# Optimization experiments

Measured on AMD Instinct MI355X. Metric: run time of the kernel, lower is better.

Reference implementation:

```python
import jax, jax.numpy as jnp
import numpy as np

HIDDEN, NH, NKV, HD = 2048, 16, 2, 128
CTX, NL, POS = 4096, 36, 3000
THETA, EPS = 1.0e6, 1e-6


def _rope_cos_sin(pos):
    inv_freq = 1.0 / (THETA ** (jnp.arange(0, HD, 2, dtype=jnp.float32) / HD))  # [HD/2]
    ang = pos * inv_freq
    ang = jnp.concatenate([ang, ang])  # [HD]
    return jnp.cos(ang), jnp.sin(ang)


def _rotate_half(x):
    x1, x2 = x[..., : HD // 2], x[..., HD // 2 :]
    return jnp.concatenate([-x2, x1], axis=-1)


def setup_inputs() -> dict:
    key = jax.random.key(0)
    ks = jax.random.split(key, 12)
    w = lambda k, shape, s=0.02: (jax.random.normal(k, shape, dtype=jnp.float32) * s)
    mask = jnp.where(jnp.arange(CTX) <= POS, 0.0, -1e9).astype(jnp.float32).reshape(1, 1, 1, CTX)
    return {
        "hidden_states": jax.random.normal(ks[0], (1, 1, HIDDEN), dtype=jnp.float32),
        "position_ids": jnp.array([POS], dtype=jnp.int64 if jax.config.jax_enable_x64 else jnp.int32),
        "causal_mask": mask,
        "current_pos": POS,
        "ln_w": jnp.ones((HIDDEN,), jnp.float32) + w(ks[1], (HIDDEN,)),
        "wq": w(ks[2], (NH * HD, HIDDEN)),
        "bq": w(ks[3], (NH * HD,)),
        "wk": w(ks[4], (NKV * HD, HIDDEN)),
        "bk": w(ks[5], (NKV * HD,)),
        "wv": w(ks[6], (NKV * HD, HIDDEN)),
        "bv": w(ks[7], (NKV * HD,)),
        "wo": w(ks[8], (HIDDEN, NH * HD)),
        "kv_cache": w(ks[9], (2 * NL, NKV, CTX, HD), 1.0),
    }


def reference(hidden_states, position_ids, causal_mask, current_pos,
              ln_w, wq, bq, wk, bk, wv, bv, wo, kv_cache):
    x = hidden_states  # [1,1,H]
    # RMSNorm
    var = jnp.mean(x * x, axis=-1, keepdims=True)
    nx = x * jax.lax.rsqrt(var + EPS) * ln_w

    # QKV projections (single token)
    t = nx[0, 0]  # [H]
    q = (wq @ t + bq).reshape(NH, HD)    # [NH, HD]
    k = (wk @ t + bk).reshape(NKV, HD)   # [NKV, HD]
    v = (wv @ t + bv).reshape(NKV, HD)

    # RoPE at current position
    cos, sin = _rope_cos_sin(jnp.float32(current_pos))
    q = q * cos + _rotate_half(q) * sin
    k = k * cos + _rotate_half(k) * sin

    # KV-cache scatter write: key at layer slot 0, value at slot NL
    kv_cache = kv_cache.at[0, :, current_pos, :].set(k)
    kv_cache = kv_cache.at[NL, :, current_pos, :].set(v)
    key_cache = kv_cache[0]    # [NKV, CTX, HD]
    value_cache = kv_cache[NL]

    # GQA attention over full cache
    rep = NH // NKV
    K = jnp.repeat(key_cache, rep, axis=0)    # [NH, CTX, HD]
    V = jnp.repeat(value_cache, rep, axis=0)
    scores = jnp.einsum("hd,hkd->hk", q, K) / jnp.sqrt(jnp.float32(HD))
    scores = scores + causal_mask[0, 0, 0]    # [NH, CTX]
    probs = jax.nn.softmax(scores, axis=-1)
    ctx = jnp.einsum("hk,hkd->hd", probs, V)  # [NH, HD]
    attn_out = (wo @ ctx.reshape(NH * HD)).reshape(1, 1, HIDDEN)

    return hidden_states + attn_out
```

## Files before the change

### kernel.cpp

```cpp
#include <hip/hip_runtime.h>
#include <hip/hip_bf16.h>
#include <math.h>

#define HIDDEN 2048
#define NH 16
#define NKV 2
#define HD 128
#define CTX 4096
#define NL 36
#define EPS 1e-6f

#define CHUNK 128
#define NCHUNKS 32
#define HPB 8
#define NATT 64

#define WS_QRAW 0
#define WS_KRAW 2048
#define WS_VRAW 2304
#define WS_TAB  2560
#define WS_PML  2688
#define WS_PACC 3712

#define RSQRT_HD 0.08838834764831845f

__device__ __forceinline__ float dot4(float4 a, float4 b) {
    return a.x*b.x + a.y*b.y + a.z*b.z + a.w*b.w;
}

__global__ __launch_bounds__(256, 1) void qkv_kernel(
    const float* __restrict__ x, const float* __restrict__ lnw,
    const float* __restrict__ wq, const float* __restrict__ bq,
    const float* __restrict__ wk, const float* __restrict__ bk,
    const float* __restrict__ wv, const float* __restrict__ bv,
    const int* __restrict__ curpos, float* __restrict__ ws)
{
    const int t = threadIdx.x;
    const int lane = t & 63, wid = t >> 6;
    const int b = blockIdx.x;

    if (b == 160) {
        if (t < 64) {
            double e = (double)t * (1.0 / 64.0);
            double invf = exp2(-19.931568569324174087 * e);
            double a = (double)curpos[0] * invf;
            a -= 6.2831853071795864769 * floor(a * 0.15915494309189533577);
            float s, c;
            sincosf((float)a, &s, &c);
            ws[WS_TAB + t] = c;
            ws[WS_TAB + 64 + t] = s;
        }
        return;
    }

    const int R0 = b * 16 + wid * 4;
    const float* wr[4]; float bias[4];
    #pragma unroll
    for (int r = 0; r < 4; ++r) {
        const int R = R0 + r;
        if (R < 2048)      { wr[r] = wq + (size_t)R * HIDDEN;            bias[r] = bq[R]; }
        else if (R < 2304) { wr[r] = wk + (size_t)(R - 2048) * HIDDEN;   bias[r] = bk[R - 2048]; }
        else               { wr[r] = wv + (size_t)(R - 2304) * HIDDEN;   bias[r] = bv[R - 2304]; }
    }

    float4 xa = ((const float4*)x)[t * 2];
    float4 xb = ((const float4*)x)[t * 2 + 1];
    float4 la = ((const float4*)lnw)[t * 2];
    float4 lb = ((const float4*)lnw)[t * 2 + 1];
    float4 u[4][8];
    #pragma unroll
    for (int r = 0; r < 4; ++r)
        #pragma unroll
        for (int j = 0; j < 8; ++j)
            u[r][j] = ((const float4*)wr[r])[j * 64 + lane];

    __shared__ float nx[HIDDEN];
    __shared__ float redS[4];
    float ss = dot4(xa, xa) + dot4(xb, xb);
    #pragma unroll
    for (int m = 32; m; m >>= 1) ss += __shfl_xor(ss, m);
    if (lane == 0) redS[wid] = ss;
    __syncthreads();
    const float inv = rsqrtf((redS[0] + redS[1] + redS[2] + redS[3]) * (1.f / HIDDEN) + EPS);
    float4 na, nb;
    na.x = xa.x * inv * la.x; na.y = xa.y * inv * la.y;
    na.z = xa.z * inv * la.z; na.w = xa.w * inv * la.w;
    nb.x = xb.x * inv * lb.x; nb.y = xb.y * inv * lb.y;
    nb.z = xb.z * inv * lb.z; nb.w = xb.w * inv * lb.w;
    ((float4*)nx)[t * 2] = na;
    ((float4*)nx)[t * 2 + 1] = nb;
    __syncthreads();

    const float4* nx4 = (const float4*)nx;
    float a[4] = {0.f, 0.f, 0.f, 0.f};
    #pragma unroll
    for (int j = 0; j < 8; ++j) {
        float4 n = nx4[j * 64 + lane];
        #pragma unroll
        for (int r = 0; r < 4; ++r) a[r] += dot4(u[r][j], n);
    }
    #pragma unroll
    for (int r = 0; r < 4; ++r)
        #pragma unroll
        for (int m = 32; m; m >>= 1) a[r] += __shfl_xor(a[r], m);
    if (lane == 0) {
        #pragma unroll
        for (int r = 0; r < 4; ++r) ws[R0 + r] = a[r] + bias[r];
    }
}

__global__ __launch_bounds__(256, 1) void attn_kernel(
    const float* __restrict__ kvc, const int* __restrict__ curpos,
    float* __restrict__ ws)
{
    const int pos = curpos[0];
    const int grp = blockIdx.x >> 5;
    const int c = blockIdx.x & 31;
    const int start = c * CHUNK;
    if (start > pos) return;
    const int nvalid = min(CHUNK, pos + 1 - start);
    const int h0 = grp * HPB;
    const float* kc = kvc + (size_t)grp * CTX * HD;
    const float* vc = kvc + (size_t)(NL * NKV + grp) * CTX * HD;

    __shared__ float tab[128];
    __shared__ float kf[HD];
    __shared__ float qr[HPB][HD];
    __shared__ float sc[HPB][CHUNK];
    __shared__ float ctxh[8][HPB][HD];

    const int t = threadIdx.x;
    const int lane = t & 63, wid = t >> 6;
    const int g16 = t >> 4, li = t & 15;
    const int half = t >> 5, q4 = t & 31;

    float tabv = 0.f;
    if (t < 128) tabv = ws[WS_TAB + t];
    float krv = 0.f, krp = 0.f;
    if (t < 128) {
        const float* kr = ws + WS_KRAW + (size_t)grp * HD;
        krv = kr[t]; krp = kr[t ^ 64];
    }
    float qv[4], qp[4];
    #pragma unroll
    for (int i = 0; i < 4; ++i) {
        int e = t + i * 256;
        int hh = e >> 7, d = e & 127;
        const float* q = ws + WS_QRAW + (size_t)(h0 + hh) * HD;
        qv[i] = q[d]; qp[i] = q[d ^ 64];
    }
    float4 fv = ((const float4*)(ws + WS_VRAW + (size_t)grp * HD))[q4];

    float4 ka[8], kb[8];
    #pragma unroll
    for (int it = 0; it < 8; ++it) {
        const int pp = start + it * 16 + g16;
        const float4* kp = (const float4*)(kc + (size_t)pp * HD + li * 8);
        ka[it] = kp[0]; kb[it] = kp[1];
    }
    float4 vv[16];
    #pragma unroll
    for (int i = 0; i < 16; ++i) {
        const int pp = start + i * 8 + half;
        vv[i] = ((const float4*)(vc + (size_t)pp * HD))[q4];
    }

    if (t < 128) tab[t] = tabv;
    __syncthreads();
    if (t < 128) {
        float r = (t < 64) ? -krp : krp;
        kf[t] = krv * tab[t & 63] + r * tab[64 + (t & 63)];
    }
    #pragma unroll
    for (int i = 0; i < 4; ++i) {
        int e = t + i * 256;
        int hh = e >> 7, d = e & 127;
        float r = (d < 64) ? -qp[i] : qp[i];
        qr[hh][d] = (qv[i] * tab[d & 63] + r * tab[64 + (d & 63)]) * RSQRT_HD;
    }
    __syncthreads();

    #pragma unroll
    for (int P = 0; P < 2; ++P) {
        float4 qa[4], qb[4];
        #pragma unroll
        for (int hh = 0; hh < 4; ++hh) {
            qa[hh] = *(const float4*)&qr[P * 4 + hh][li * 8];
            qb[hh] = *(const float4*)&qr[P * 4 + hh][li * 8 + 4];
        }
        #pragma unroll
        for (int it = 0; it < 8; ++it) {
            const int pl = it * 16 + g16;
            float4 A = ka[it], B = kb[it];
            if (start + pl == pos) {
                A = *(const float4*)&kf[li * 8];
                B = *(const float4*)&kf[li * 8 + 4];
            }
            float s0 = dot4(qa[0], A) + dot4(qb[0], B);
            float s1 = dot4(qa[1], A) + dot4(qb[1], B);
            float s2 = dot4(qa[2], A) + dot4(qb[2], B);
            float s3 = dot4(qa[3], A) + dot4(qb[3], B);
            #pragma unroll
            for (int m = 1; m < 16; m <<= 1) {
                s0 += __shfl_xor(s0, m); s1 += __shfl_xor(s1, m);
                s2 += __shfl_xor(s2, m); s3 += __shfl_xor(s3, m);
            }
            if (pl < nvalid && li == 0) {
                sc[P * 4 + 0][pl] = s0; sc[P * 4 + 1][pl] = s1;
                sc[P * 4 + 2][pl] = s2; sc[P * 4 + 3][pl] = s3;
            }
        }
    }
    #pragma unroll
    for (int i = 0; i < 4; ++i) {
        int e = t + i * 256;
        int hh = e >> 7, pl = e & 127;
        if (pl >= nvalid) sc[hh][pl] = 0.f;
    }
    __syncthreads();

    #pragma unroll
    for (int pass = 0; pass < 2; ++pass) {
        const int hh = wid + pass * 4;
        float m = -INFINITY;
        for (int pp = lane; pp < nvalid; pp += 64) m = fmaxf(m, sc[hh][pp]);
        #pragma unroll
        for (int mm = 32; mm; mm >>= 1) m = fmaxf(m, __shfl_xor(m, mm));
        float l = 0.f;
        for (int pp = lane; pp < nvalid; pp += 64) {
            float e = expf(sc[hh][pp] - m);
            sc[hh][pp] = e;
            l += e;
        }
        #pragma unroll
        for (int mm = 32; mm; mm >>= 1) l += __shfl_xor(l, mm);
        if (lane == 0) {
            ws[WS_PML + ((size_t)(h0 + hh) * NCHUNKS + c) * 2]     = m;
            ws[WS_PML + ((size_t)(h0 + hh) * NCHUNKS + c) * 2 + 1] = l;
        }
    }
    __syncthreads();

    #pragma unroll
    for (int P = 0; P < 2; ++P) {
        float4 a[4];
        #pragma unroll
        for (int hh = 0; hh < 4; ++hh) a[hh] = make_float4(0.f, 0.f, 0.f, 0.f);
        #pragma unroll
        for (int i = 0; i < 16; ++i) {
            const int pl = i * 8 + half;
            float4 xv = (start + pl == pos) ? fv : vv[i];
            #pragma unroll
            for (int hh = 0; hh < 4; ++hh) {
                float w = sc[P * 4 + hh][pl];
                a[hh].x += w * xv.x; a[hh].y += w * xv.y;
                a[hh].z += w * xv.z; a[hh].w += w * xv.w;
            }
        }
        #pragma unroll
        for (int hh = 0; hh < 4; ++hh)
            *(float4*)&ctxh[half][P * 4 + hh][q4 * 4] = a[hh];
    }
    __syncthreads();

    #pragma unroll
    for (int i = 0; i < 4; ++i) {
        int e = t + i * 256;
        int hh = e >> 7, d = e & 127;
        float s = 0.f;
        #pragma unroll
        for (int hf = 0; hf < 8; ++hf) s += ctxh[hf][hh][d];
        ws[WS_PACC + ((size_t)(h0 + hh) * NCHUNKS + c) * 128 + d] = s;
    }
}

__global__ __launch_bounds__(256, 1) void out_kernel(
    const float* __restrict__ wo, const float* __restrict__ hidden,
    const float* __restrict__ ws, const int* __restrict__ curpos,
    float* __restrict__ out)
{
    const int t = threadIdx.x;
    const int lane = t & 63, wid = t >> 6;

    const int row0 = blockIdx.x * 8 + wid * 2;
    const float4* w04 = (const float4*)(wo + (size_t)row0 * HIDDEN);
    const float4* w14 = (const float4*)(wo + (size_t)(row0 + 1) * HIDDEN);
    float4 u[8], v[8];
    #pragma unroll
    for (int j = 0; j < 8; ++j) { u[j] = w04[j * 64 + lane]; v[j] = w14[j * 64 + lane]; }

    __shared__ float ctx[HIDDEN];
    const int pos = curpos[0];
    const int nc = pos / CHUNK + 1;
    const int h = t >> 4, sub = t & 15;
    float M = -INFINITY;
    for (int c2 = 0; c2 < nc; ++c2)
        M = fmaxf(M, ws[WS_PML + ((size_t)h * NCHUNKS + c2) * 2]);
    float L = 0.f;
    float4 acc0 = make_float4(0.f,0.f,0.f,0.f), acc1 = make_float4(0.f,0.f,0.f,0.f);
    for (int c2 = 0; c2 < nc; ++c2) {
        float mm = ws[WS_PML + ((size_t)h * NCHUNKS + c2) * 2];
        float ll = ws[WS_PML + ((size_t)h * NCHUNKS + c2) * 2 + 1];
        float w = expf(mm - M);
        L += w * ll;
        const float4* pa = (const float4*)(ws + WS_PACC + ((size_t)h * NCHUNKS + c2) * 128 + sub * 8);
        float4 p0 = pa[0], p1 = pa[1];
        acc0.x += w*p0.x; acc0.y += w*p0.y; acc0.z += w*p0.z; acc0.w += w*p0.w;
        acc1.x += w*p1.x; acc1.y += w*p1.y; acc1.z += w*p1.z; acc1.w += w*p1.w;
    }
    float invL = 1.f / L;
    acc0.x *= invL; acc0.y *= invL; acc0.z *= invL; acc0.w *= invL;
    acc1.x *= invL; acc1.y *= invL; acc1.z *= invL; acc1.w *= invL;
    *(float4*)&ctx[h * HD + sub * 8]     = acc0;
    *(float4*)&ctx[h * HD + sub * 8 + 4] = acc1;
    __syncthreads();

    const float4* c4 = (const float4*)ctx;
    float a0 = 0.f, a1 = 0.f;
    #pragma unroll
    for (int j = 0; j < 8; ++j) {
        float4 n = c4[j * 64 + lane];
        a0 += dot4(u[j], n);
        a1 += dot4(v[j], n);
    }
    #pragma unroll
    for (int m = 32; m; m >>= 1) { a0 += __shfl_xor(a0, m); a1 += __shfl_xor(a1, m); }
    if (lane == 0) {
        out[row0]     = hidden[row0]     + a0;
        out[row0 + 1] = hidden[row0 + 1] + a1;
    }
}

extern "C" void kernel_launch(void* const* d_in, const int* in_sizes, int n_in,
                              void* d_out, int out_size, void* d_ws, size_t ws_size,
                              hipStream_t stream)
{
    const float* hidden = (const float*)d_in[0];
    const int*   cur    = (const int*)d_in[3];
    const float* lnw    = (const float*)d_in[4];
    const float* wq     = (const float*)d_in[5];
    const float* bq     = (const float*)d_in[6];
    const float* wk     = (const float*)d_in[7];
    const float* bk     = (const float*)d_in[8];
    const float* wv     = (const float*)d_in[9];
    const float* bv     = (const float*)d_in[10];
    const float* wo     = (const float*)d_in[11];
    const float* kv     = (const float*)d_in[12];
    float* ws  = (float*)d_ws;
    float* out = (float*)d_out;

    qkv_kernel<<<dim3(161), dim3(256), 0, stream>>>(hidden, lnw, wq, bq, wk, bk, wv, bv, cur, ws);
    attn_kernel<<<dim3(NATT), dim3(256), 0, stream>>>(kv, cur, ws);
    out_kernel<<<dim3(256), dim3(256), 0, stream>>>(wo, hidden, ws, cur, out);
}
```

Baseline: 43.57 us.

## Fuse QKV, attention, and output projection into one cooperative kernel with grid syncs

Replaces the three kernel launches with a single cooperative kernel of 256 blocks that uses grid-wide syncs between the QKV projection, the chunked attention, and the output projection. QKV rows are redistributed across all 256 blocks. Each block prefetches its Wo rows into registers before the second grid sync, so that weight load overlaps the attention phase. The goal is to remove launch gaps and tail latency between kernels, at the cost of grid sync overhead and higher register and shared-memory pressure per block.

```diff
diff --git a/kernel.cpp b/kernel.cpp
--- a/kernel.cpp
+++ b/kernel.cpp
@@ -1,6 +1,9 @@
 #include <hip/hip_runtime.h>
 #include <hip/hip_bf16.h>
+#include <hip/hip_cooperative_groups.h>
 #include <math.h>
+
+namespace cg = cooperative_groups;
 
 #define HIDDEN 2048
 #define NH 16
@@ -14,6 +17,7 @@
 #define NCHUNKS 32
 #define HPB 8
 #define NATT 64
+#define NBLK 256
 
 #define WS_QRAW 0
 #define WS_KRAW 2048
@@ -28,54 +32,71 @@
     return a.x*b.x + a.y*b.y + a.z*b.z + a.w*b.w;
 }
 
-__global__ __launch_bounds__(256, 1) void qkv_kernel(
+__global__ __launch_bounds__(256, 1) void fused_kernel(
     const float* __restrict__ x, const float* __restrict__ lnw,
     const float* __restrict__ wq, const float* __restrict__ bq,
     const float* __restrict__ wk, const float* __restrict__ bk,
     const float* __restrict__ wv, const float* __restrict__ bv,
-    const int* __restrict__ curpos, float* __restrict__ ws)
+    const float* __restrict__ wo, const float* __restrict__ kvc,
+    const int* __restrict__ curpos, float* __restrict__ ws,
+    float* __restrict__ out)
 {
+    cg::grid_group grid = cg::this_grid();
     const int t = threadIdx.x;
     const int lane = t & 63, wid = t >> 6;
     const int b = blockIdx.x;
-
-    if (b == 160) {
-        if (t < 64) {
-            double e = (double)t * (1.0 / 64.0);
-            double invf = exp2(-19.931568569324174087 * e);
-            double a = (double)curpos[0] * invf;
-            a -= 6.2831853071795864769 * floor(a * 0.15915494309189533577);
-            float s, c;
-            sincosf((float)a, &s, &c);
-            ws[WS_TAB + t] = c;
-            ws[WS_TAB + 64 + t] = s;
-        }
-        return;
-    }
-
-    const int R0 = b * 16 + wid * 4;
-    const float* wr[4]; float bias[4];
-    #pragma unroll
-    for (int r = 0; r < 4; ++r) {
-        const int R = R0 + r;
-        if (R < 2048)      { wr[r] = wq + (size_t)R * HIDDEN;            bias[r] = bq[R]; }
-        else if (R < 2304) { wr[r] = wk + (size_t)(R - 2048) * HIDDEN;   bias[r] = bk[R - 2048]; }
-        else               { wr[r] = wv + (size_t)(R - 2304) * HIDDEN;   bias[r] = bv[R - 2304]; }
+    const int pos = curpos[0];
+
+    __shared__ float nx[HIDDEN];
+    __shared__ float redS[4];
+    __shared__ float tab[128];
+    __shared__ float kf[HD];
+    __shared__ float qr[HPB][HD];
+    __shared__ float sc[HPB][CHUNK];
+    __shared__ float ctxh[8][HPB][HD];
+    __shared__ float ctx2[HIDDEN];
+
+    const int nrows = (wid < 2) ? 3 : 2;
+    int Rw[3];
+    Rw[0] = b * 8 + wid * 2;
+    Rw[1] = Rw[0] + 1;
+    Rw[2] = 2048 + b * 2 + wid;
+
+    const float* wr[3]; float bias[3];
+    #pragma unroll
+    for (int r = 0; r < 3; ++r) {
+        const int R = Rw[r];
+        if (R < 2048)      { wr[r] = wq + (size_t)R * HIDDEN;          bias[r] = bq[R]; }
+        else if (R < 2304) { wr[r] = wk + (size_t)(R - 2048) * HIDDEN; bias[r] = bk[R - 2048]; }
+        else               { wr[r] = wv + (size_t)(R - 2304) * HIDDEN; bias[r] = bv[R - 2304]; }
     }
 
     float4 xa = ((const float4*)x)[t * 2];
     float4 xb = ((const float4*)x)[t * 2 + 1];
     float4 la = ((const float4*)lnw)[t * 2];
     float4 lb = ((const float4*)lnw)[t * 2 + 1];
-    float4 u[4][8];
-    #pragma unroll
-    for (int r = 0; r < 4; ++r)
-        #pragma unroll
-        for (int j = 0; j < 8; ++j)
-            u[r][j] = ((const float4*)wr[r])[j * 64 + lane];
-
-    __shared__ float nx[HIDDEN];
-    __shared__ float redS[4];
+    float4 u0[8], u1[8], u2[8];
+    #pragma unroll
+    for (int j = 0; j < 8; ++j) u0[j] = ((const float4*)wr[0])[j * 64 + lane];
+    #pragma unroll
+    for (int j = 0; j < 8; ++j) u1[j] = ((const float4*)wr[1])[j * 64 + lane];
+    if (wid < 2) {
+        #pragma unroll
+        for (int j = 0; j < 8; ++j) u2[j] = ((const float4*)wr[2])[j * 64 + lane];
+    }
+
+    if (b == 0 && wid == 3) {
+        const int i = lane;
+        double e = (double)i * (1.0 / 64.0);
+        double invf = exp2(-19.931568569324174087 * e);
+        double a = (double)pos * invf;
+        a -= 6.2831853071795864769 * floor(a * 0.15915494309189533577);
+        float s, c;
+        sincosf((float)a, &s, &c);
+        ws[WS_TAB + i] = c;
+        ws[WS_TAB + 64 + i] = s;
+    }
+
     float ss = dot4(xa, xa) + dot4(xb, xb);
     #pragma unroll
     for (int m = 32; m; m >>= 1) ss += __shfl_xor(ss, m);
@@ -92,230 +113,214 @@
     __syncthreads();
 
     const float4* nx4 = (const float4*)nx;
-    float a[4] = {0.f, 0.f, 0.f, 0.f};
+    float acc[3] = {0.f, 0.f, 0.f};
     #pragma unroll
     for (int j = 0; j < 8; ++j) {
         float4 n = nx4[j * 64 + lane];
-        #pragma unroll
-        for (int r = 0; r < 4; ++r) a[r] += dot4(u[r][j], n);
-    }
-    #pragma unroll
-    for (int r = 0; r < 4; ++r)
-        #pragma unroll
-        for (int m = 32; m; m >>= 1) a[r] += __shfl_xor(a[r], m);
+        acc[0] += dot4(u0[j], n);
+        acc[1] += dot4(u1[j], n);
+        if (wid < 2) acc[2] += dot4(u2[j], n);
+    }
+    #pragma unroll
+    for (int r = 0; r < 3; ++r)
+        #pragma unroll
+        for (int m = 32; m; m >>= 1) acc[r] += __shfl_xor(acc[r], m);
     if (lane == 0) {
-        #pragma unroll
-        for (int r = 0; r < 4; ++r) ws[R0 + r] = a[r] + bias[r];
-    }
-}
-
-__global__ __launch_bounds__(256, 1) void attn_kernel(
-    const float* __restrict__ kvc, const int* __restrict__ curpos,
-    float* __restrict__ ws)
-{
-    const int pos = curpos[0];
-    const int grp = blockIdx.x >> 5;
-    const int c = blockIdx.x & 31;
-    const int start = c * CHUNK;
-    if (start > pos) return;
-    const int nvalid = min(CHUNK, pos + 1 - start);
-    const int h0 = grp * HPB;
-    const float* kc = kvc + (size_t)grp * CTX * HD;
-    const float* vc = kvc + (size_t)(NL * NKV + grp) * CTX * HD;
-
-    __shared__ float tab[128];
-    __shared__ float kf[HD];
-    __shared__ float qr[HPB][HD];
-    __shared__ float sc[HPB][CHUNK];
-    __shared__ float ctxh[8][HPB][HD];
-
-    const int t = threadIdx.x;
-    const int lane = t & 63, wid = t >> 6;
-    const int g16 = t >> 4, li = t & 15;
-    const int half = t >> 5, q4 = t & 31;
-
-    float tabv = 0.f;
-    if (t < 128) tabv = ws[WS_TAB + t];
-    float krv = 0.f, krp = 0.f;
-    if (t < 128) {
-        const float* kr = ws + WS_KRAW + (size_t)grp * HD;
-        krv = kr[t]; krp = kr[t ^ 64];
-    }
-    float qv[4], qp[4];
-    #pragma unroll
-    for (int i = 0; i < 4; ++i) {
-        int e = t + i * 256;
-        int hh = e >> 7, d = e & 127;
-        const float* q = ws + WS_QRAW + (size_t)(h0 + hh) * HD;
-        qv[i] = q[d]; qp[i] = q[d ^ 64];
-    }
-    float4 fv = ((const float4*)(ws + WS_VRAW + (size_t)grp * HD))[q4];
-
-    float4 ka[8], kb[8];
-    #pragma unroll
-    for (int it = 0; it < 8; ++it) {
-        const int pp = start + it * 16 + g16;
-        const float4* kp = (const float4*)(kc + (size_t)pp * HD + li * 8);
-        ka[it] = kp[0]; kb[it] = kp[1];
-    }
-    float4 vv[16];
-    #pragma unroll
-    for (int i = 0; i < 16; ++i) {
-        const int pp = start + i * 8 + half;
-        vv[i] = ((const float4*)(vc + (size_t)pp * HD))[q4];
-    }
-
-    if (t < 128) tab[t] = tabv;
-    __syncthreads();
-    if (t < 128) {
-        float r = (t < 64) ? -krp : krp;
-        kf[t] = krv * tab[t & 63] + r * tab[64 + (t & 63)];
-    }
-    #pragma unroll
-    for (int i = 0; i < 4; ++i) {
-        int e = t + i * 256;
-        int hh = e >> 7, d = e & 127;
-        float r = (d < 64) ? -qp[i] : qp[i];
-        qr[hh][d] = (qv[i] * tab[d & 63] + r * tab[64 + (d & 63)]) * RSQRT_HD;
-    }
-    __syncthreads();
-
-    #pragma unroll
-    for (int P = 0; P < 2; ++P) {
-        float4 qa[4], qb[4];
-        #pragma unroll
-        for (int hh = 0; hh < 4; ++hh) {
-            qa[hh] = *(const float4*)&qr[P * 4 + hh][li * 8];
-            qb[hh] = *(const float4*)&qr[P * 4 + hh][li * 8 + 4];
-        }
+        ws[Rw[0]] = acc[0] + bias[0];
+        ws[Rw[1]] = acc[1] + bias[1];
+        if (wid < 2) ws[Rw[2]] = acc[2] + bias[2];
+    }
+
+    __threadfence();
+    grid.sync();
+
+    const int grp = b >> 5, c = b & 31, start = c * CHUNK;
+    const bool attnRole = (b < NATT) && (start <= pos);
+
+    if (attnRole) {
+        const int nvalid = min(CHUNK, pos + 1 - start);
+        const int h0 = grp * HPB;
+        const float* kc = kvc + (size_t)grp * CTX * HD;
+        const float* vc = kvc + (size_t)(NL * NKV + grp) * CTX * HD;
+        const int g16 = t >> 4, li = t & 15;
+        const int half = t >> 5, q4 = t & 31;
+
+        float tabv = 0.f, krv = 0.f, krp = 0.f;
+        if (t < 128) {
+            tabv = ws[WS_TAB + t];
+            const float* kr = ws + WS_KRAW + (size_t)grp * HD;
+            krv = kr[t]; krp = kr[t ^ 64];
+        }
+        float qv[4], qp[4];
+        #pragma unroll
+        for (int i = 0; i < 4; ++i) {
+            int e = t + i * 256;
+            int hh = e >> 7, d = e & 127;
+            const float* q = ws + WS_QRAW + (size_t)(h0 + hh) * HD;
+            qv[i] = q[d]; qp[i] = q[d ^ 64];
+        }
+        float4 fv = ((const float4*)(ws + WS_VRAW + (size_t)grp * HD))[q4];
+
+        float4 ka[8], kb[8];
         #pragma unroll
         for (int it = 0; it < 8; ++it) {
-            const int pl = it * 16 + g16;
-            float4 A = ka[it], B = kb[it];
-            if (start + pl == pos) {
-                A = *(const float4*)&kf[li * 8];
-                B = *(const float4*)&kf[li * 8 + 4];
-            }
-            float s0 = dot4(qa[0], A) + dot4(qb[0], B);
-            float s1 = dot4(qa[1], A) + dot4(qb[1], B);
-            float s2 = dot4(qa[2], A) + dot4(qb[2], B);
-            float s3 = dot4(qa[3], A) + dot4(qb[3], B);
-            #pragma unroll
-            for (int m = 1; m < 16; m <<= 1) {
-                s0 += __shfl_xor(s0, m); s1 += __shfl_xor(s1, m);
-                s2 += __shfl_xor(s2, m); s3 += __shfl_xor(s3, m);
-            }
-            if (pl < nvalid && li == 0) {
-                sc[P * 4 + 0][pl] = s0; sc[P * 4 + 1][pl] = s1;
-                sc[P * 4 + 2][pl] = s2; sc[P * 4 + 3][pl] = s3;
-            }
-        }
-    }
-    #pragma unroll
-    for (int i = 0; i < 4; ++i) {
-        int e = t + i * 256;
-        int hh = e >> 7, pl = e & 127;
-        if (pl >= nvalid) sc[hh][pl] = 0.f;
-    }
-    __syncthreads();
-
-    #pragma unroll
-    for (int pass = 0; pass < 2; ++pass) {
-        const int hh = wid + pass * 4;
-        float m = -INFINITY;
-        for (int pp = lane; pp < nvalid; pp += 64) m = fmaxf(m, sc[hh][pp]);
-        #pragma unroll
-        for (int mm = 32; mm; mm >>= 1) m = fmaxf(m, __shfl_xor(m, mm));
-        float l = 0.f;
-        for (int pp = lane; pp < nvalid; pp += 64) {
-            float e = expf(sc[hh][pp] - m);
-            sc[hh][pp] = e;
-            l += e;
-        }
-        #pragma unroll
-        for (int mm = 32; mm; mm >>= 1) l += __shfl_xor(l, mm);
-        if (lane == 0) {
-            ws[WS_PML + ((size_t)(h0 + hh) * NCHUNKS + c) * 2]     = m;
-            ws[WS_PML + ((size_t)(h0 + hh) * NCHUNKS + c) * 2 + 1] = l;
-        }
-    }
-    __syncthreads();
-
-    #pragma unroll
-    for (int P = 0; P < 2; ++P) {
-        float4 a[4];
-        #pragma unroll
-        for (int hh = 0; hh < 4; ++hh) a[hh] = make_float4(0.f, 0.f, 0.f, 0.f);
+            const int pp = start + it * 16 + g16;
+            const float4* kp = (const float4*)(kc + (size_t)pp * HD + li * 8);
+            ka[it] = kp[0]; kb[it] = kp[1];
+        }
+        float4 vv[16];
         #pragma unroll
         for (int i = 0; i < 16; ++i) {
-            const int pl = i * 8 + half;
-            float4 xv = (start + pl == pos) ? fv : vv[i];
+            const int pp = start + i * 8 + half;
+            vv[i] = ((const float4*)(vc + (size_t)pp * HD))[q4];
+        }
+
+        if (t < 128) tab[t] = tabv;
+        __syncthreads();
+        if (t < 128) {
+            float r = (t < 64) ? -krp : krp;
+            kf[t] = krv * tab[t & 63] + r * tab[64 + (t & 63)];
+        }
+        #pragma unroll
+        for (int i = 0; i < 4; ++i) {
+            int e = t + i * 256;
+            int hh = e >> 7, d = e & 127;
+            float r = (d < 64) ? -qp[i] : qp[i];
+            qr[hh][d] = (qv[i] * tab[d & 63] + r * tab[64 + (d & 63)]) * RSQRT_HD;
+        }
+        __syncthreads();
+
+        #pragma unroll
+        for (int P = 0; P < 2; ++P) {
+            float4 qa[4], qb[4];
             #pragma unroll
             for (int hh = 0; hh < 4; ++hh) {
-                float w = sc[P * 4 + hh][pl];
-                a[hh].x += w * xv.x; a[hh].y += w * xv.y;
-                a[hh].z += w * xv.z; a[hh].w += w * xv.w;
-            }
-        }
-        #pragma unroll
-        for (int hh = 0; hh < 4; ++hh)
-            *(float4*)&ctxh[half][P * 4 + hh][q4 * 4] = a[hh];
-    }
-    __syncthreads();
-
-    #pragma unroll
-    for (int i = 0; i < 4; ++i) {
-        int e = t + i * 256;
-        int hh = e >> 7, d = e & 127;
-        float s = 0.f;
-        #pragma unroll
-        for (int hf = 0; hf < 8; ++hf) s += ctxh[hf][hh][d];
-        ws[WS_PACC + ((size_t)(h0 + hh) * NCHUNKS + c) * 128 + d] = s;
-    }
-}
-
-__global__ __launch_bounds__(256, 1) void out_kernel(
-    const float* __restrict__ wo, const float* __restrict__ hidden,
-    const float* __restrict__ ws, const int* __restrict__ curpos,
-    float* __restrict__ out)
-{
-    const int t = threadIdx.x;
-    const int lane = t & 63, wid = t >> 6;
-
-    const int row0 = blockIdx.x * 8 + wid * 2;
+                qa[hh] = *(const float4*)&qr[P * 4 + hh][li * 8];
+                qb[hh] = *(const float4*)&qr[P * 4 + hh][li * 8 + 4];
+            }
+            #pragma unroll
+            for (int it = 0; it < 8; ++it) {
+                const int pl = it * 16 + g16;
+                float4 A = ka[it], B = kb[it];
+                if (start + pl == pos) {
+                    A = *(const float4*)&kf[li * 8];
+                    B = *(const float4*)&kf[li * 8 + 4];
+                }
+                float s0 = dot4(qa[0], A) + dot4(qb[0], B);
+                float s1 = dot4(qa[1], A) + dot4(qb[1], B);
+                float s2 = dot4(qa[2], A) + dot4(qb[2], B);
+                float s3 = dot4(qa[3], A) + dot4(qb[3], B);
+                #pragma unroll
+                for (int m = 1; m < 16; m <<= 1) {
+                    s0 += __shfl_xor(s0, m); s1 += __shfl_xor(s1, m);
+                    s2 += __shfl_xor(s2, m); s3 += __shfl_xor(s3, m);
+                }
+                if (pl < nvalid && li == 0) {
+                    sc[P * 4 + 0][pl] = s0; sc[P * 4 + 1][pl] = s1;
+                    sc[P * 4 + 2][pl] = s2; sc[P * 4 + 3][pl] = s3;
+                }
+            }
+        }
+        #pragma unroll
+        for (int i = 0; i < 4; ++i) {
+            int e = t + i * 256;
+            int hh = e >> 7, pl = e & 127;
+            if (pl >= nvalid) sc[hh][pl] = 0.f;
+        }
+        __syncthreads();
+
+        #pragma unroll
+        for (int pass = 0; pass < 2; ++pass) {
+            const int hh = wid + pass * 4;
+            float m = -INFINITY;
+            for (int pp = lane; pp < nvalid; pp += 64) m = fmaxf(m, sc[hh][pp]);
+            #pragma unroll
+            for (int mm = 32; mm; mm >>= 1) m = fmaxf(m, __shfl_xor(m, mm));
+            float l = 0.f;
+            for (int pp = lane; pp < nvalid; pp += 64) {
+                float e = expf(sc[hh][pp] - m);
+                sc[hh][pp] = e;
+                l += e;
+            }
+            #pragma unroll
+            for (int mm = 32; mm; mm >>= 1) l += __shfl_xor(l, mm);
+            if (lane == 0) {
+                ws[WS_PML + ((size_t)(h0 + hh) * NCHUNKS + c) * 2]     = m;
+                ws[WS_PML + ((size_t)(h0 + hh) * NCHUNKS + c) * 2 + 1] = l;
+            }
+        }
+        __syncthreads();
+
+        #pragma unroll
+        for (int P = 0; P < 2; ++P) {
+            float4 a[4];
+            #pragma unroll
+            for (int hh = 0; hh < 4; ++hh) a[hh] = make_float4(0.f, 0.f, 0.f, 0.f);
+            #pragma unroll
+            for (int i = 0; i < 16; ++i) {
+                const int pl = i * 8 + half;
+                float4 xv = (start + pl == pos) ? fv : vv[i];
+                #pragma unroll
+                for (int hh = 0; hh < 4; ++hh) {
+                    float w = sc[P * 4 + hh][pl];
+                    a[hh].x += w * xv.x; a[hh].y += w * xv.y;
+                    a[hh].z += w * xv.z; a[hh].w += w * xv.w;
+                }
+            }
+            #pragma unroll
+            for (int hh = 0; hh < 4; ++hh)
+                *(float4*)&ctxh[half][P * 4 + hh][q4 * 4] = a[hh];
+        }
+        __syncthreads();
+
+        #pragma unroll
+        for (int i = 0; i < 4; ++i) {
+            int e = t + i * 256;
+            int hh = e >> 7, d = e & 127;
+            float s = 0.f;
+            #pragma unroll
+            for (int hf = 0; hf < 8; ++hf) s += ctxh[hf][hh][d];
+            ws[WS_PACC + ((size_t)(h0 + hh) * NCHUNKS + c) * 128 + d] = s;
+        }
+    }
+
+    const int row0 = b * 8 + wid * 2;
     const float4* w04 = (const float4*)(wo + (size_t)row0 * HIDDEN);
     const float4* w14 = (const float4*)(wo + (size_t)(row0 + 1) * HIDDEN);
     float4 u[8], v[8];
     #pragma unroll
     for (int j = 0; j < 8; ++j) { u[j] = w04[j * 64 + lane]; v[j] = w14[j * 64 + lane]; }
 
-    __shared__ float ctx[HIDDEN];
-    const int pos = curpos[0];
-    const int nc = pos / CHUNK + 1;
-    const int h = t >> 4, sub = t & 15;
-    float M = -INFINITY;
-    for (int c2 = 0; c2 < nc; ++c2)
-        M = fmaxf(M, ws[WS_PML + ((size_t)h * NCHUNKS + c2) * 2]);
-    float L = 0.f;
-    float4 acc0 = make_float4(0.f,0.f,0.f,0.f), acc1 = make_float4(0.f,0.f,0.f,0.f);
-    for (int c2 = 0; c2 < nc; ++c2) {
-        float mm = ws[WS_PML + ((size_t)h * NCHUNKS + c2) * 2];
-        float ll = ws[WS_PML + ((size_t)h * NCHUNKS + c2) * 2 + 1];
-        float w = expf(mm - M);
-        L += w * ll;
-        const float4* pa = (const float4*)(ws + WS_PACC + ((size_t)h * NCHUNKS + c2) * 128 + sub * 8);
-        float4 p0 = pa[0], p1 = pa[1];
-        acc0.x += w*p0.x; acc0.y += w*p0.y; acc0.z += w*p0.z; acc0.w += w*p0.w;
-        acc1.x += w*p1.x; acc1.y += w*p1.y; acc1.z += w*p1.z; acc1.w += w*p1.w;
-    }
-    float invL = 1.f / L;
-    acc0.x *= invL; acc0.y *= invL; acc0.z *= invL; acc0.w *= invL;
-    acc1.x *= invL; acc1.y *= invL; acc1.z *= invL; acc1.w *= invL;
-    *(float4*)&ctx[h * HD + sub * 8]     = acc0;
-    *(float4*)&ctx[h * HD + sub * 8 + 4] = acc1;
+    __threadfence();
+    grid.sync();
+
+    {
+        const int nc = pos / CHUNK + 1;
+        const int h = t >> 4, sub = t & 15;
+        float M = -INFINITY;
+        for (int c2 = 0; c2 < nc; ++c2)
+            M = fmaxf(M, ws[WS_PML + ((size_t)h * NCHUNKS + c2) * 2]);
+        float L = 0.f;
+        float4 acc0 = make_float4(0.f,0.f,0.f,0.f), acc1 = make_float4(0.f,0.f,0.f,0.f);
+        for (int c2 = 0; c2 < nc; ++c2) {
+            float mm = ws[WS_PML + ((size_t)h * NCHUNKS + c2) * 2];
+            float ll = ws[WS_PML + ((size_t)h * NCHUNKS + c2) * 2 + 1];
+            float w = expf(mm - M);
+            L += w * ll;
+            const float4* pa = (const float4*)(ws + WS_PACC + ((size_t)h * NCHUNKS + c2) * 128 + sub * 8);
+            float4 p0 = pa[0], p1 = pa[1];
+            acc0.x += w*p0.x; acc0.y += w*p0.y; acc0.z += w*p0.z; acc0.w += w*p0.w;
+            acc1.x += w*p1.x; acc1.y += w*p1.y; acc1.z += w*p1.z; acc1.w += w*p1.w;
+        }
+        float invL = 1.f / L;
+        acc0.x *= invL; acc0.y *= invL; acc0.z *= invL; acc0.w *= invL;
+        acc1.x *= invL; acc1.y *= invL; acc1.z *= invL; acc1.w *= invL;
+        *(float4*)&ctx2[h * HD + sub * 8]     = acc0;
+        *(float4*)&ctx2[h * HD + sub * 8 + 4] = acc1;
+    }
     __syncthreads();
 
-    const float4* c4 = (const float4*)ctx;
+    const float4* c4 = (const float4*)ctx2;
     float a0 = 0.f, a1 = 0.f;
     #pragma unroll
     for (int j = 0; j < 8; ++j) {
@@ -326,8 +331,8 @@
     #pragma unroll
     for (int m = 32; m; m >>= 1) { a0 += __shfl_xor(a0, m); a1 += __shfl_xor(a1, m); }
     if (lane == 0) {
-        out[row0]     = hidden[row0]     + a0;
-        out[row0 + 1] = hidden[row0 + 1] + a1;
+        out[row0]     = x[row0]     + a0;
+        out[row0 + 1] = x[row0 + 1] + a1;
     }
 }
 
@@ -349,7 +354,10 @@
     float* ws  = (float*)d_ws;
     float* out = (float*)d_out;
 
-    qkv_kernel<<<dim3(161), dim3(256), 0, stream>>>(hidden, lnw, wq, bq, wk, bk, wv, bv, cur, ws);
-    attn_kernel<<<dim3(NATT), dim3(256), 0, stream>>>(kv, cur, ws);
-    out_kernel<<<dim3(256), dim3(256), 0, stream>>>(wo, hidden, ws, cur, out);
+    void* args[] = { (void*)&hidden, (void*)&lnw, (void*)&wq, (void*)&bq,
+                     (void*)&wk, (void*)&bk, (void*)&wv, (void*)&bv,
+                     (void*)&wo, (void*)&kv, (void*)&cur, (void*)&ws,
+                     (void*)&out };
+    hipLaunchCooperativeKernel((void*)fused_kernel, dim3(NBLK), dim3(256),
+                               args, 0, stream);
 }
```

New measurement: 137.3 us. 3.15x slower.

## Fuse attention and output projection with flag-based inter-block sync

Applied to the files above, without the earlier changes.

Merges the attention and output-projection kernels into one launch of 256 blocks. The first 64 blocks compute partial attention and publish per-block ready flags with release stores. Every block prefetches its Wo rows, then spins on the flags before combining the partial softmax results and doing the projection. The flags are reset by the table-building block of the QKV kernel, which is also retiled to 2 rows per wave over 321 blocks. This removes one kernel launch and overlaps the Wo loads with attention, but it relies on all 256 blocks being co-resident and adds spin-wait overhead.

```diff
diff --git a/kernel.cpp b/kernel.cpp
--- a/kernel.cpp
+++ b/kernel.cpp
@@ -21,6 +21,7 @@
 #define WS_TAB  2560
 #define WS_PML  2688
 #define WS_PACC 3712
+#define WS_FLAG 69248
 
 #define RSQRT_HD 0.08838834764831845f
 
@@ -37,10 +38,10 @@
 {
     const int t = threadIdx.x;
     const int lane = t & 63, wid = t >> 6;
-    const int b = blockIdx.x;
-
-    if (b == 160) {
+
+    if (blockIdx.x == 320) {
         if (t < 64) {
+            ((int*)(ws + WS_FLAG))[t * 32] = 0;
             double e = (double)t * (1.0 / 64.0);
             double invf = exp2(-19.931568569324174087 * e);
             double a = (double)curpos[0] * invf;
@@ -53,35 +54,36 @@
         return;
     }
 
-    const int R0 = b * 16 + wid * 4;
-    const float* wr[4]; float bias[4];
-    #pragma unroll
-    for (int r = 0; r < 4; ++r) {
-        const int R = R0 + r;
-        if (R < 2048)      { wr[r] = wq + (size_t)R * HIDDEN;            bias[r] = bq[R]; }
-        else if (R < 2304) { wr[r] = wk + (size_t)(R - 2048) * HIDDEN;   bias[r] = bk[R - 2048]; }
-        else               { wr[r] = wv + (size_t)(R - 2304) * HIDDEN;   bias[r] = bv[R - 2304]; }
-    }
-
+    const int R0 = blockIdx.x * 8 + wid * 2;
+    const float *w0, *w1; float b0, b1; float *dst0, *dst1;
+    {
+        int R = R0;
+        if (R < 2048)      { w0 = wq + (size_t)R * HIDDEN;            b0 = bq[R];   dst0 = ws + WS_QRAW + R; }
+        else if (R < 2304) { int r = R - 2048; w0 = wk + (size_t)r * HIDDEN; b0 = bk[r]; dst0 = ws + WS_KRAW + r; }
+        else               { int r = R - 2304; w0 = wv + (size_t)r * HIDDEN; b0 = bv[r]; dst0 = ws + WS_VRAW + r; }
+        R = R0 + 1;
+        if (R < 2048)      { w1 = wq + (size_t)R * HIDDEN;            b1 = bq[R];   dst1 = ws + WS_QRAW + R; }
+        else if (R < 2304) { int r = R - 2048; w1 = wk + (size_t)r * HIDDEN; b1 = bk[r]; dst1 = ws + WS_KRAW + r; }
+        else               { int r = R - 2304; w1 = wv + (size_t)r * HIDDEN; b1 = bv[r]; dst1 = ws + WS_VRAW + r; }
+    }
+    const float4* w04 = (const float4*)w0;
+    const float4* w14 = (const float4*)w1;
+    float4 u[8], v[8];
+    #pragma unroll
+    for (int j = 0; j < 8; ++j) { u[j] = w04[j * 64 + lane]; v[j] = w14[j * 64 + lane]; }
+
+    __shared__ float nx[HIDDEN];
+    __shared__ float red[4];
     float4 xa = ((const float4*)x)[t * 2];
     float4 xb = ((const float4*)x)[t * 2 + 1];
+    float ss = dot4(xa, xa) + dot4(xb, xb);
+    #pragma unroll
+    for (int m = 32; m; m >>= 1) ss += __shfl_xor(ss, m);
+    if (lane == 0) red[wid] = ss;
+    __syncthreads();
+    float inv = rsqrtf((red[0] + red[1] + red[2] + red[3]) * (1.f / HIDDEN) + EPS);
     float4 la = ((const float4*)lnw)[t * 2];
     float4 lb = ((const float4*)lnw)[t * 2 + 1];
-    float4 u[4][8];
-    #pragma unroll
-    for (int r = 0; r < 4; ++r)
-        #pragma unroll
-        for (int j = 0; j < 8; ++j)
-            u[r][j] = ((const float4*)wr[r])[j * 64 + lane];
-
-    __shared__ float nx[HIDDEN];
-    __shared__ float redS[4];
-    float ss = dot4(xa, xa) + dot4(xb, xb);
-    #pragma unroll
-    for (int m = 32; m; m >>= 1) ss += __shfl_xor(ss, m);
-    if (lane == 0) redS[wid] = ss;
-    __syncthreads();
-    const float inv = rsqrtf((redS[0] + redS[1] + redS[2] + redS[3]) * (1.f / HIDDEN) + EPS);
     float4 na, nb;
     na.x = xa.x * inv * la.x; na.y = xa.y * inv * la.y;
     na.z = xa.z * inv * la.z; na.w = xa.w * inv * la.w;
@@ -92,230 +94,235 @@
     __syncthreads();
 
     const float4* nx4 = (const float4*)nx;
-    float a[4] = {0.f, 0.f, 0.f, 0.f};
+    float a0 = 0.f, a1 = 0.f;
     #pragma unroll
     for (int j = 0; j < 8; ++j) {
         float4 n = nx4[j * 64 + lane];
-        #pragma unroll
-        for (int r = 0; r < 4; ++r) a[r] += dot4(u[r][j], n);
-    }
-    #pragma unroll
-    for (int r = 0; r < 4; ++r)
-        #pragma unroll
-        for (int m = 32; m; m >>= 1) a[r] += __shfl_xor(a[r], m);
-    if (lane == 0) {
-        #pragma unroll
-        for (int r = 0; r < 4; ++r) ws[R0 + r] = a[r] + bias[r];
-    }
+        a0 += dot4(u[j], n);
+        a1 += dot4(v[j], n);
+    }
+    #pragma unroll
+    for (int m = 32; m; m >>= 1) { a0 += __shfl_xor(a0, m); a1 += __shfl_xor(a1, m); }
+    if (lane == 0) { *dst0 = a0 + b0; *dst1 = a1 + b1; }
 }
 
-__global__ __launch_bounds__(256, 1) void attn_kernel(
-    const float* __restrict__ kvc, const int* __restrict__ curpos,
-    float* __restrict__ ws)
+__global__ __launch_bounds__(256, 1) void attn_out_kernel(
+    const float* __restrict__ wo, const float* __restrict__ kvc,
+    const int* __restrict__ curpos, const float* __restrict__ hidden,
+    float* __restrict__ ws, float* __restrict__ out)
 {
+    const int t = threadIdx.x;
+    const int lane = t & 63, wid = t >> 6;
+    const int b = blockIdx.x;
     const int pos = curpos[0];
-    const int grp = blockIdx.x >> 5;
-    const int c = blockIdx.x & 31;
-    const int start = c * CHUNK;
-    if (start > pos) return;
-    const int nvalid = min(CHUNK, pos + 1 - start);
-    const int h0 = grp * HPB;
-    const float* kc = kvc + (size_t)grp * CTX * HD;
-    const float* vc = kvc + (size_t)(NL * NKV + grp) * CTX * HD;
+    int* flg = (int*)(ws + WS_FLAG);
 
     __shared__ float tab[128];
     __shared__ float kf[HD];
     __shared__ float qr[HPB][HD];
     __shared__ float sc[HPB][CHUNK];
     __shared__ float ctxh[8][HPB][HD];
-
-    const int t = threadIdx.x;
-    const int lane = t & 63, wid = t >> 6;
-    const int g16 = t >> 4, li = t & 15;
-    const int half = t >> 5, q4 = t & 31;
-
-    float tabv = 0.f;
-    if (t < 128) tabv = ws[WS_TAB + t];
-    float krv = 0.f, krp = 0.f;
-    if (t < 128) {
-        const float* kr = ws + WS_KRAW + (size_t)grp * HD;
-        krv = kr[t]; krp = kr[t ^ 64];
-    }
-    float qv[4], qp[4];
-    #pragma unroll
-    for (int i = 0; i < 4; ++i) {
-        int e = t + i * 256;
-        int hh = e >> 7, d = e & 127;
-        const float* q = ws + WS_QRAW + (size_t)(h0 + hh) * HD;
-        qv[i] = q[d]; qp[i] = q[d ^ 64];
-    }
-    float4 fv = ((const float4*)(ws + WS_VRAW + (size_t)grp * HD))[q4];
-
-    float4 ka[8], kb[8];
-    #pragma unroll
-    for (int it = 0; it < 8; ++it) {
-        const int pp = start + it * 16 + g16;
-        const float4* kp = (const float4*)(kc + (size_t)pp * HD + li * 8);
-        ka[it] = kp[0]; kb[it] = kp[1];
-    }
-    float4 vv[16];
-    #pragma unroll
-    for (int i = 0; i < 16; ++i) {
-        const int pp = start + i * 8 + half;
-        vv[i] = ((const float4*)(vc + (size_t)pp * HD))[q4];
-    }
-
-    if (t < 128) tab[t] = tabv;
-    __syncthreads();
-    if (t < 128) {
-        float r = (t < 64) ? -krp : krp;
-        kf[t] = krv * tab[t & 63] + r * tab[64 + (t & 63)];
-    }
-    #pragma unroll
-    for (int i = 0; i < 4; ++i) {
-        int e = t + i * 256;
-        int hh = e >> 7, d = e & 127;
-        float r = (d < 64) ? -qp[i] : qp[i];
-        qr[hh][d] = (qv[i] * tab[d & 63] + r * tab[64 + (d & 63)]) * RSQRT_HD;
-    }
-    __syncthreads();
-
-    #pragma unroll
-    for (int P = 0; P < 2; ++P) {
-        float4 qa[4], qb[4];
-        #pragma unroll
-        for (int hh = 0; hh < 4; ++hh) {
-            qa[hh] = *(const float4*)&qr[P * 4 + hh][li * 8];
-            qb[hh] = *(const float4*)&qr[P * 4 + hh][li * 8 + 4];
+    __shared__ float ctx2[HIDDEN];
+
+    if (b < NATT) {
+        const int grp = b >> 5, c = b & 31, start = c * CHUNK;
+        if (start <= pos) {
+            const int nvalid = min(CHUNK, pos + 1 - start);
+            const int h0 = grp * HPB;
+            const float* kc = kvc + (size_t)grp * CTX * HD;
+            const float* vc = kvc + (size_t)(NL * NKV + grp) * CTX * HD;
+            const int g16 = t >> 4, li = t & 15;
+            const int half = t >> 5, q4 = t & 31;
+
+            float tabv = 0.f, krv = 0.f, krp = 0.f;
+            if (t < 128) {
+                tabv = ws[WS_TAB + t];
+                const float* kr = ws + WS_KRAW + (size_t)grp * HD;
+                krv = kr[t]; krp = kr[t ^ 64];
+            }
+            float qv[4], qp[4];
+            #pragma unroll
+            for (int i = 0; i < 4; ++i) {
+                int e = t + i * 256;
+                int hh = e >> 7, d = e & 127;
+                const float* q = ws + WS_QRAW + (size_t)(h0 + hh) * HD;
+                qv[i] = q[d]; qp[i] = q[d ^ 64];
+            }
+            float4 fv = ((const float4*)(ws + WS_VRAW + (size_t)grp * HD))[q4];
+
+            float4 ka[8], kb[8];
+            #pragma unroll
+            for (int it = 0; it < 8; ++it) {
+                const int pp = start + it * 16 + g16;
+                const float4* kp = (const float4*)(kc + (size_t)pp * HD + li * 8);
+                ka[it] = kp[0]; kb[it] = kp[1];
+            }
+            float4 vv[16];
+            #pragma unroll
+            for (int i = 0; i < 16; ++i) {
+                const int pp = start + i * 8 + half;
+                vv[i] = ((const float4*)(vc + (size_t)pp * HD))[q4];
+            }
+
+            if (t < 128) tab[t] = tabv;
+            __syncthreads();
+            if (t < 128) {
+                float r = (t < 64) ? -krp : krp;
+                kf[t] = krv * tab[t & 63] + r * tab[64 + (t & 63)];
+            }
+            #pragma unroll
+            for (int i = 0; i < 4; ++i) {
+                int e = t + i * 256;
+                int hh = e >> 7, d = e & 127;
+                float r = (d < 64) ? -qp[i] : qp[i];
+                qr[hh][d] = (qv[i] * tab[d & 63] + r * tab[64 + (d & 63)]) * RSQRT_HD;
+            }
+            __syncthreads();
+
+            #pragma unroll
+            for (int P = 0; P < 2; ++P) {
+                float4 qa[4], qb[4];
+                #pragma unroll
+                for (int hh = 0; hh < 4; ++hh) {
+                    qa[hh] = *(const float4*)&qr[P * 4 + hh][li * 8];
+                    qb[hh] = *(const float4*)&qr[P * 4 + hh][li * 8 + 4];
+                }
+                #pragma unroll
+                for (int it = 0; it < 8; ++it) {
+                    const int pl = it * 16 + g16;
+                    float4 A = ka[it], B = kb[it];
+                    if (start + pl == pos) {
+                        A = *(const float4*)&kf[li * 8];
+                        B = *(const float4*)&kf[li * 8 + 4];
+                    }
+                    float s0 = dot4(qa[0], A) + dot4(qb[0], B);
+                    float s1 = dot4(qa[1], A) + dot4(qb[1], B);
+                    float s2 = dot4(qa[2], A) + dot4(qb[2], B);
+                    float s3 = dot4(qa[3], A) + dot4(qb[3], B);
+                    #pragma unroll
+                    for (int m = 1; m < 16; m <<= 1) {
+                        s0 += __shfl_xor(s0, m); s1 += __shfl_xor(s1, m);
+                        s2 += __shfl_xor(s2, m); s3 += __shfl_xor(s3, m);
+                    }
+                    if (pl < nvalid && li == 0) {
+                        sc[P * 4 + 0][pl] = s0; sc[P * 4 + 1][pl] = s1;
+                        sc[P * 4 + 2][pl] = s2; sc[P * 4 + 3][pl] = s3;
+                    }
+                }
+            }
+            #pragma unroll
+            for (int i = 0; i < 4; ++i) {
+                int e = t + i * 256;
+                int hh = e >> 7, pl = e & 127;
+                if (pl >= nvalid) sc[hh][pl] = 0.f;
+            }
+            __syncthreads();
+
+            #pragma unroll
+            for (int pass = 0; pass < 2; ++pass) {
+                const int hh = wid + pass * 4;
+                float m = -INFINITY;
+                for (int pp = lane; pp < nvalid; pp += 64) m = fmaxf(m, sc[hh][pp]);
+                #pragma unroll
+                for (int mm = 32; mm; mm >>= 1) m = fmaxf(m, __shfl_xor(m, mm));
+                float l = 0.f;
+                for (int pp = lane; pp < nvalid; pp += 64) {
+                    float e = expf(sc[hh][pp] - m);
+                    sc[hh][pp] = e;
+                    l += e;
+                }
+                #pragma unroll
+                for (int mm = 32; mm; mm >>= 1) l += __shfl_xor(l, mm);
+                if (lane == 0) {
+                    ws[WS_PML + ((size_t)(h0 + hh) * NCHUNKS + c) * 2]     = m;
+                    ws[WS_PML + ((size_t)(h0 + hh) * NCHUNKS + c) * 2 + 1] = l;
+                }
+            }
+            __syncthreads();
+
+            #pragma unroll
+            for (int P = 0; P < 2; ++P) {
+                float4 a[4];
+                #pragma unroll
+                for (int hh = 0; hh < 4; ++hh) a[hh] = make_float4(0.f, 0.f, 0.f, 0.f);
+                #pragma unroll
+                for (int i = 0; i < 16; ++i) {
+                    const int pl = i * 8 + half;
+                    float4 xv = (start + pl == pos) ? fv : vv[i];
+                    #pragma unroll
+                    for (int hh = 0; hh < 4; ++hh) {
+                        float w = sc[P * 4 + hh][pl];
+                        a[hh].x += w * xv.x; a[hh].y += w * xv.y;
+                        a[hh].z += w * xv.z; a[hh].w += w * xv.w;
+                    }
+                }
+                #pragma unroll
+                for (int hh = 0; hh < 4; ++hh)
+                    *(float4*)&ctxh[half][P * 4 + hh][q4 * 4] = a[hh];
+            }
+            __syncthreads();
+
+            #pragma unroll
+            for (int i = 0; i < 4; ++i) {
+                int e = t + i * 256;
+                int hh = e >> 7, d = e & 127;
+                float s = 0.f;
+                #pragma unroll
+                for (int hf = 0; hf < 8; ++hf) s += ctxh[hf][hh][d];
+                ws[WS_PACC + ((size_t)(h0 + hh) * NCHUNKS + c) * 128 + d] = s;
+            }
         }
-        #pragma unroll
-        for (int it = 0; it < 8; ++it) {
-            const int pl = it * 16 + g16;
-            float4 A = ka[it], B = kb[it];
-            if (start + pl == pos) {
-                A = *(const float4*)&kf[li * 8];
-                B = *(const float4*)&kf[li * 8 + 4];
-            }
-            float s0 = dot4(qa[0], A) + dot4(qb[0], B);
-            float s1 = dot4(qa[1], A) + dot4(qb[1], B);
-            float s2 = dot4(qa[2], A) + dot4(qb[2], B);
-            float s3 = dot4(qa[3], A) + dot4(qb[3], B);
-            #pragma unroll
-            for (int m = 1; m < 16; m <<= 1) {
-                s0 += __shfl_xor(s0, m); s1 += __shfl_xor(s1, m);
-                s2 += __shfl_xor(s2, m); s3 += __shfl_xor(s3, m);
-            }
-            if (pl < nvalid && li == 0) {
-                sc[P * 4 + 0][pl] = s0; sc[P * 4 + 1][pl] = s1;
-                sc[P * 4 + 2][pl] = s2; sc[P * 4 + 3][pl] = s3;
-            }
-        }
-    }
-    #pragma unroll
-    for (int i = 0; i < 4; ++i) {
-        int e = t + i * 256;
-        int hh = e >> 7, pl = e & 127;
-        if (pl >= nvalid) sc[hh][pl] = 0.f;
-    }
-    __syncthreads();
-
-    #pragma unroll
-    for (int pass = 0; pass < 2; ++pass) {
-        const int hh = wid + pass * 4;
-        float m = -INFINITY;
-        for (int pp = lane; pp < nvalid; pp += 64) m = fmaxf(m, sc[hh][pp]);
-        #pragma unroll
-        for (int mm = 32; mm; mm >>= 1) m = fmaxf(m, __shfl_xor(m, mm));
-        float l = 0.f;
-        for (int pp = lane; pp < nvalid; pp += 64) {
-            float e = expf(sc[hh][pp] - m);
-            sc[hh][pp] = e;
-            l += e;
-        }
-        #pragma unroll
-        for (int mm = 32; mm; mm >>= 1) l += __shfl_xor(l, mm);
-        if (lane == 0) {
-            ws[WS_PML + ((size_t)(h0 + hh) * NCHUNKS + c) * 2]     = m;
-            ws[WS_PML + ((size_t)(h0 + hh) * NCHUNKS + c) * 2 + 1] = l;
-        }
-    }
-    __syncthreads();
-
-    #pragma unroll
-    for (int P = 0; P < 2; ++P) {
-        float4 a[4];
-        #pragma unroll
-        for (int hh = 0; hh < 4; ++hh) a[hh] = make_float4(0.f, 0.f, 0.f, 0.f);
-        #pragma unroll
-        for (int i = 0; i < 16; ++i) {
-            const int pl = i * 8 + half;
-            float4 xv = (start + pl == pos) ? fv : vv[i];
-            #pragma unroll
-            for (int hh = 0; hh < 4; ++hh) {
-                float w = sc[P * 4 + hh][pl];
-                a[hh].x += w * xv.x; a[hh].y += w * xv.y;
-                a[hh].z += w * xv.z; a[hh].w += w * xv.w;
-            }
-        }
-        #pragma unroll
-        for (int hh = 0; hh < 4; ++hh)
-            *(float4*)&ctxh[half][P * 4 + hh][q4 * 4] = a[hh];
-    }
-    __syncthreads();
-
-    #pragma unroll
-    for (int i = 0; i < 4; ++i) {
-        int e = t + i * 256;
-        int hh = e >> 7, d = e & 127;
-        float s = 0.f;
-        #pragma unroll
-        for (int hf = 0; hf < 8; ++hf) s += ctxh[hf][hh][d];
-        ws[WS_PACC + ((size_t)(h0 + hh) * NCHUNKS + c) * 128 + d] = s;
-    }
-}
-
-__global__ __launch_bounds__(256, 1) void out_kernel(
-    const float* __restrict__ wo, const float* __restrict__ hidden,
-    const float* __restrict__ ws, const int* __restrict__ curpos,
-    float* __restrict__ out)
-{
-    const int t = threadIdx.x;
-    const int lane = t & 63, wid = t >> 6;
-
-    const int row0 = blockIdx.x * 8 + wid * 2;
+        __syncthreads();
+        __threadfence();
+        if (t == 0)
+            __hip_atomic_store(&flg[b * 32], 1, __ATOMIC_RELEASE, __HIP_MEMORY_SCOPE_AGENT);
+    }
+
+    const int row0 = b * 8 + wid * 2;
     const float4* w04 = (const float4*)(wo + (size_t)row0 * HIDDEN);
     const float4* w14 = (const float4*)(wo + (size_t)(row0 + 1) * HIDDEN);
     float4 u[8], v[8];
     #pragma unroll
     for (int j = 0; j < 8; ++j) { u[j] = w04[j * 64 + lane]; v[j] = w14[j * 64 + lane]; }
 
-    __shared__ float ctx[HIDDEN];
-    const int pos = curpos[0];
-    const int nc = pos / CHUNK + 1;
-    const int h = t >> 4, sub = t & 15;
-    float M = -INFINITY;
-    for (int c2 = 0; c2 < nc; ++c2)
-        M = fmaxf(M, ws[WS_PML + ((size_t)h * NCHUNKS + c2) * 2]);
-    float L = 0.f;
-    float4 acc0 = make_float4(0.f,0.f,0.f,0.f), acc1 = make_float4(0.f,0.f,0.f,0.f);
-    for (int c2 = 0; c2 < nc; ++c2) {
-        float mm = ws[WS_PML + ((size_t)h * NCHUNKS + c2) * 2];
-        float ll = ws[WS_PML + ((size_t)h * NCHUNKS + c2) * 2 + 1];
-        float w = expf(mm - M);
-        L += w * ll;
-        const float4* pa = (const float4*)(ws + WS_PACC + ((size_t)h * NCHUNKS + c2) * 128 + sub * 8);
-        float4 p0 = pa[0], p1 = pa[1];
-        acc0.x += w*p0.x; acc0.y += w*p0.y; acc0.z += w*p0.z; acc0.w += w*p0.w;
-        acc1.x += w*p1.x; acc1.y += w*p1.y; acc1.z += w*p1.z; acc1.w += w*p1.w;
-    }
-    float invL = 1.f / L;
-    acc0.x *= invL; acc0.y *= invL; acc0.z *= invL; acc0.w *= invL;
-    acc1.x *= invL; acc1.y *= invL; acc1.z *= invL; acc1.w *= invL;
-    *(float4*)&ctx[h * HD + sub * 8]     = acc0;
-    *(float4*)&ctx[h * HD + sub * 8 + 4] = acc1;
+    if (wid == 0) {
+        while (true) {
+            int f = __hip_atomic_load(&flg[lane * 32], __ATOMIC_ACQUIRE,
+                                      __HIP_MEMORY_SCOPE_AGENT);
+            if (__all(f == 1)) break;
+            __builtin_amdgcn_s_sleep(32);
+        }
+    }
     __syncthreads();
-
-    const float4* c4 = (const float4*)ctx;
+    __threadfence();
+
+    {
+        const int nc = pos / CHUNK + 1;
+        const int h = t >> 4, sub = t & 15;
+        float M = -INFINITY;
+        for (int c2 = 0; c2 < nc; ++c2)
+            M = fmaxf(M, ws[WS_PML + ((size_t)h * NCHUNKS + c2) * 2]);
+        float L = 0.f;
+        float4 acc0 = make_float4(0.f,0.f,0.f,0.f), acc1 = make_float4(0.f,0.f,0.f,0.f);
+        for (int c2 = 0; c2 < nc; ++c2) {
+            float mm = ws[WS_PML + ((size_t)h * NCHUNKS + c2) * 2];
+            float ll = ws[WS_PML + ((size_t)h * NCHUNKS + c2) * 2 + 1];
+            float w = expf(mm - M);
+            L += w * ll;
+            const float4* pa = (const float4*)(ws + WS_PACC + ((size_t)h * NCHUNKS + c2) * 128 + sub * 8);
+            float4 p0 = pa[0], p1 = pa[1];
+            acc0.x += w*p0.x; acc0.y += w*p0.y; acc0.z += w*p0.z; acc0.w += w*p0.w;
+            acc1.x += w*p1.x; acc1.y += w*p1.y; acc1.z += w*p1.z; acc1.w += w*p1.w;
+        }
+        float invL = 1.f / L;
+        acc0.x *= invL; acc0.y *= invL; acc0.z *= invL; acc0.w *= invL;
+        acc1.x *= invL; acc1.y *= invL; acc1.z *= invL; acc1.w *= invL;
+        *(float4*)&ctx2[h * HD + sub * 8]     = acc0;
+        *(float4*)&ctx2[h * HD + sub * 8 + 4] = acc1;
+    }
+    __syncthreads();
+
+    const float4* c4 = (const float4*)ctx2;
     float a0 = 0.f, a1 = 0.f;
     #pragma unroll
     for (int j = 0; j < 8; ++j) {
@@ -349,7 +356,6 @@
     float* ws  = (float*)d_ws;
     float* out = (float*)d_out;
 
-    qkv_kernel<<<dim3(161), dim3(256), 0, stream>>>(hidden, lnw, wq, bq, wk, bk, wv, bv, cur, ws);
-    attn_kernel<<<dim3(NATT), dim3(256), 0, stream>>>(kv, cur, ws);
-    out_kernel<<<dim3(256), dim3(256), 0, stream>>>(wo, hidden, ws, cur, out);
+    qkv_kernel<<<dim3(321), dim3(256), 0, stream>>>(hidden, lnw, wq, bq, wk, bk, wv, bv, cur, ws);
+    attn_out_kernel<<<dim3(256), dim3(256), 0, stream>>>(wo, kv, cur, hidden, ws, out);
 }
```

Measured after the change: 89.58 us. 2.06x slower.
